# Kernel tuning notes

Hardware: AMD Instinct MI355X
Metric: run time of the kernel (lower is better)

The kernel has to match this reference:

```python
import jax, jax.numpy as jnp
import numpy as np
import math

H = 16
LORA_SCALING = 16 / 8  # alpha / r
NEG_INF = -1e30

def _alibi_slopes(n_heads):
    start = 2.0 ** (-(2.0 ** (-(math.log2(n_heads) - 3))))
    return jnp.asarray([start * start ** i for i in range(n_heads)], dtype=jnp.float32)

def setup_inputs() -> dict:
    key = jax.random.key(0)
    ks = jax.random.split(key, 11)
    B, T, E, r = 4, 2048, 1024, 8
    d = {
        'x':  jax.random.normal(ks[0], (B, T, E), jnp.float32),
        'Wq': jax.random.normal(ks[1], (E, E), jnp.float32) * (E ** -0.5),
        'Aq': jax.random.normal(ks[2], (E, r), jnp.float32) * 0.01,
        'Bq': jax.random.normal(ks[3], (r, E), jnp.float32) * 0.01,
        'Wk': jax.random.normal(ks[4], (E, E), jnp.float32) * (E ** -0.5),
        'Ak': jax.random.normal(ks[5], (E, r), jnp.float32) * 0.01,
        'Bk': jax.random.normal(ks[6], (r, E), jnp.float32) * 0.01,
        'Wv': jax.random.normal(ks[7], (E, E), jnp.float32) * (E ** -0.5),
        'Av': jax.random.normal(ks[8], (E, r), jnp.float32) * 0.01,
        'Bv': jax.random.normal(ks[9], (r, E), jnp.float32) * 0.01,
        'Wp': jax.random.normal(ks[10], (E, E), jnp.float32) * (E ** -0.5),
    }
    return d

def _lora(x, W, A, Bm):
    # nn.Linear: x @ W.T ; LoRA: x @ B.T @ A.T * scaling
    return x @ W.T + ((x @ Bm.T) @ A.T) * LORA_SCALING

def reference(x, Wq, Aq, Bq, Wk, Ak, Bk, Wv, Av, Bv, Wp):
    B, T, E = x.shape
    dh = E // H
    q = _lora(x, Wq, Aq, Bq).reshape(B, T, H, dh).transpose(0, 2, 1, 3)  # [B,H,T,dh]
    k = _lora(x, Wk, Ak, Bk).reshape(B, T, H, dh).transpose(0, 2, 1, 3)
    v = _lora(x, Wv, Av, Bv).reshape(B, T, H, dh).transpose(0, 2, 1, 3)
    s = jnp.einsum('bhqd,bhkd->bhqk', q, k) / jnp.sqrt(jnp.float32(dh))
    i = jnp.arange(T)[:, None]
    j = jnp.arange(T)[None, :]
    slopes = _alibi_slopes(H)
    bias = slopes[:, None, None] * (i - j).astype(jnp.float32)  # [H,T,T]
    s = s + bias[None]
    s = jnp.where(j[None, None] <= i[None, None], s, NEG_INF)  # causal mask
    out = jnp.einsum('bhqk,bhkd->bhqd', jax.nn.softmax(s, axis=-1), v)
    out = out.transpose(0, 2, 1, 3).reshape(B, T, E)
    return out @ Wp.T  # dropout is identity in eval
```

## Files before the change

### kernel.cpp

```cpp
#include <hip/hip_runtime.h>

typedef unsigned short u16;
typedef unsigned int u32;
typedef u16  u16x8 __attribute__((ext_vector_type(8)));
typedef u16  u16x4 __attribute__((ext_vector_type(4)));
typedef u32  u32x4 __attribute__((ext_vector_type(4)));
typedef __bf16 bf16x2 __attribute__((ext_vector_type(2)));
typedef __bf16 bf16x8 __attribute__((ext_vector_type(8)));
typedef float f32x4 __attribute__((ext_vector_type(4)));
typedef float f32x16 __attribute__((ext_vector_type(16)));

__constant__ int KBW[16]  = {0,1,1,2,3,5,7,10,14,20,28,40,56,80,113,160};

__constant__ unsigned char RANKTBL[256] = {
  0xBF,0xCF,0xDF,0xEF,0xFF,
  0xBE,0xCE,0xDE,0xEE,0xFE,
  0xAE,0xAF,
  0xAD,0xBD,0xCD,0xDD,0xED,0xFD,
  0xAC,0xBC,0xCC,0xDC,0xEC,0xFC,
  0xAB,0xBB,0xCB,0xDB,0xEB,0xFB,
  0xAA,0xBA,0xCA,0xDA,0xEA,0xFA,
  0x9A,0x9B,0x9C,0x9D,0x9E,0x9F,
  0x99,0xA9,0xB9,0xC9,0xD9,0xE9,0xF9,
  0x98,0xA8,0xB8,0xC8,0xD8,0xE8,0xF8,
  0x97,0xA7,0xB7,0xC7,0xD7,0xE7,0xF7,
  0x87,0x88,0x89,0x8A,0x8B,0x8C,0x8D,0x8E,0x8F,
  0x86,0x96,0xA6,0xB6,0xC6,0xD6,0xE6,0xF6,
  0x85,0x95,0xA5,0xB5,0xC5,0xD5,0xE5,0xF5,
  0x75,0x76,0x77,0x78,0x79,0x7A,0x7B,0x7C,0x7D,0x7E,0x7F,
  0x74,0x84,0x94,0xA4,0xB4,0xC4,0xD4,0xE4,0xF4,
  0x63,0x64,0x65,0x66,0x67,0x68,0x69,0x6A,0x6B,0x6C,0x6D,0x6E,0x6F,
  0x73,0x83,0x93,0xA3,0xB3,0xC3,0xD3,0xE3,0xF3,
  0x52,0x53,0x54,0x55,0x56,0x57,0x58,0x59,0x5A,0x5B,0x5C,0x5D,0x5E,0x5F,
  0x62,0x72,0x82,0x92,0xA2,0xB2,0xC2,0xD2,0xE2,0xF2,
  0x41,0x42,0x43,0x44,0x45,0x46,0x47,0x48,0x49,0x4A,0x4B,0x4C,0x4D,0x4E,0x4F,
  0x51,0x61,0x71,0x81,0x91,0xA1,0xB1,0xC1,0xD1,0xE1,0xF1,
  0x31,0x32,0x33,0x34,0x35,0x36,0x37,0x38,0x39,0x3A,0x3B,0x3C,0x3D,0x3E,0x3F,
  0x10,0x11,0x12,0x13,0x14,0x15,0x16,0x17,0x18,0x19,0x1A,0x1B,0x1C,0x1D,0x1E,0x1F,
  0x20,0x21,0x22,0x23,0x24,0x25,0x26,0x27,0x28,0x29,0x2A,0x2B,0x2C,0x2D,0x2E,0x2F,
  0x30,0x40,0x50,0x60,0x70,0x80,0x90,0xA0,0xB0,0xC0,0xD0,0xE0,0xF0,
  0x00,0x01,0x02,0x03,0x04,0x05,0x06,0x07,0x08,0x09,0x0A,0x0B,0x0C,0x0D,0x0E,0x0F
};

static __device__ __forceinline__ u16 f2bf(float f) {
  unsigned int u = __float_as_uint(f);
  u += 0x7FFFu + ((u >> 16) & 1u);
  return (u16)(u >> 16);
}

static __device__ __forceinline__ u32 packbf(float a, float b) {
  bf16x2 t;
  t[0] = (__bf16)a;
  t[1] = (__bf16)b;
  return __builtin_bit_cast(u32, t);
}

static __device__ __forceinline__ f32x4 mfma16(bf16x8 a, bf16x8 b, f32x4 c) {
  return __builtin_amdgcn_mfma_f32_16x16x32_bf16(a, b, c, 0, 0, 0);
}
static __device__ __forceinline__ f32x16 mfma32(bf16x8 a, bf16x8 b, f32x16 c) {
  return __builtin_amdgcn_mfma_f32_32x32x16_bf16(a, b, c, 0, 0, 0);
}

static __device__ __forceinline__ void gload16(const void* g, void* lds) {
  __builtin_amdgcn_global_load_lds(
      (const __attribute__((address_space(1))) unsigned int*)g,
      (__attribute__((address_space(3))) unsigned int*)lds, 16, 0, 0);
}

__global__ __launch_bounds__(256) void k_castfold(
    const float* __restrict__ x, u16* __restrict__ xb,
    const float* __restrict__ Wq, const float* __restrict__ Aq, const float* __restrict__ Bq,
    const float* __restrict__ Wk, const float* __restrict__ Ak, const float* __restrict__ Bk,
    const float* __restrict__ Wv, const float* __restrict__ Av, const float* __restrict__ Bv,
    const float* __restrict__ Wp, u16* __restrict__ wqkv, u16* __restrict__ wp) {
  const int bid = (int)blockIdx.x;
  if (bid < 4096) {
    size_t i = (size_t)bid * 256 + threadIdx.x;
    const float4* p = reinterpret_cast<const float4*>(x) + i * 2;
    float4 a = p[0], b = p[1];
    u16x8 r;
    r[0] = f2bf(a.x); r[1] = f2bf(a.y); r[2] = f2bf(a.z); r[3] = f2bf(a.w);
    r[4] = f2bf(b.x); r[5] = f2bf(b.y); r[6] = f2bf(b.z); r[7] = f2bf(b.w);
    *reinterpret_cast<u16x8*>(xb + i * 8) = r;
    return;
  }
  int n = bid - 4096;
  int widx = n >> 10, nr = n & 1023;
  const float *W, *A, *Bm; u16* dst;
  if (widx == 0)      { W = Wq; A = Aq; Bm = Bq; dst = wqkv; }
  else if (widx == 1) { W = Wk; A = Ak; Bm = Bk; dst = wqkv + (1 << 20); }
  else if (widx == 2) { W = Wv; A = Av; Bm = Bv; dst = wqkv + (2 << 20); }
  else                { W = Wp; A = nullptr; Bm = nullptr; dst = wp; }
  int e0 = threadIdx.x * 4;
  float4 w = *reinterpret_cast<const float4*>(W + (size_t)nr * 1024 + e0);
  if (widx < 3) {
    float acx = 0.f, acy = 0.f, acz = 0.f, acw = 0.f;
#pragma unroll
    for (int r = 0; r < 8; r++) {
      float ar = A[nr * 8 + r];
      float4 bm = *reinterpret_cast<const float4*>(Bm + (size_t)r * 1024 + e0);
      acx += ar * bm.x; acy += ar * bm.y; acz += ar * bm.z; acw += ar * bm.w;
    }
    w.x += 2.0f * acx; w.y += 2.0f * acy; w.z += 2.0f * acz; w.w += 2.0f * acw;
  }
  u16x4 r4; r4[0] = f2bf(w.x); r4[1] = f2bf(w.y); r4[2] = f2bf(w.z); r4[3] = f2bf(w.w);
  *reinterpret_cast<u16x4*>(dst + (size_t)nr * 1024 + e0) = r4;
}

template<int OUTF32>
__global__ __launch_bounds__(512) void k_gemm256(const u16* __restrict__ Ag,
                                                 const u16* __restrict__ Bg,
                                                 void* __restrict__ C,
                                                 int K, int N, int lda, int gx) {
  __shared__ __align__(16) u16 As[2][16384];
  __shared__ __align__(16) u16 Bs[2][16384];
  const int tid = threadIdx.x;
  const int wid = tid >> 6, lane = tid & 63;
  const int l15 = lane & 15, lg = lane >> 4;
  const int wr = wid >> 2, wc = wid & 3;
  const int nwg = gridDim.x, cpx = nwg >> 3;
  const int bid = (int)blockIdx.x;
  const int sid = (bid & 7) * cpx + (bid >> 3);
  const int m0 = (sid % gx) * 256, n0 = (sid / gx) * 256;

  const int lrow = lane >> 3;
  const int lslot = lane & 7;

  f32x4 acc[8][4];
#pragma unroll
  for (int i = 0; i < 8; i++)
#pragma unroll
    for (int j = 0; j < 4; j++) acc[i][j] = (f32x4)0.0f;

  auto stA = [&](int d, int t, int i) {
    int row = i * 64 + wid * 8 + lrow;
    int sc = (lslot ^ (row & 7)) << 3;
    gload16(Ag + (size_t)(m0 + row) * lda + t * 64 + sc, &As[d][(i * 64 + wid * 8) * 64]);
  };
  auto stB = [&](int d, int t, int i) {
    int row = i * 64 + wid * 8 + lrow;
    int sc = (lslot ^ (row & 7)) << 3;
    gload16(Bg + (size_t)(n0 + row) * K + t * 64 + sc, &Bs[d][(i * 64 + wid * 8) * 64]);
  };
  auto ldsA = [&](int d, int m, int kk) {
    int rr = wr * 128 + m * 16 + l15;
    return *reinterpret_cast<const bf16x8*>(&As[d][rr * 64 + (((kk * 4 + lg) ^ (rr & 7)) << 3)]);
  };
  auto ldsB = [&](int d, int n, int kk) {
    int rr = wc * 64 + n * 16 + l15;
    return *reinterpret_cast<const bf16x8*>(&Bs[d][rr * 64 + (((kk * 4 + lg) ^ (rr & 7)) << 3)]);
  };

#define MIDBAR do { asm volatile("s_barrier" ::: "memory"); \
                    asm volatile("s_waitcnt lgkmcnt(0)" ::: "memory"); } while (0)
#define ENDBAR asm volatile("s_barrier" ::: "memory")

  const int nt = K >> 6;
  stA(0, 0, 0); stA(0, 0, 1); stA(0, 0, 2); stA(0, 0, 3);
  stB(0, 0, 0); stB(0, 0, 1); stB(0, 0, 2); stB(0, 0, 3);
  if (nt > 1) { stB(1, 1, 0); stB(1, 1, 1); stB(1, 1, 2); stB(1, 1, 3); }
  asm volatile("s_waitcnt vmcnt(4)" ::: "memory");
  asm volatile("s_barrier" ::: "memory");

  bf16x8 fa[4][2], fbA[2][2], fbB[2][2];
  for (int t = 0; t < nt; ++t) {
    const int d = t & 1;
    const bool s1 = (t + 1 < nt), s2 = (t + 2 < nt);
#pragma unroll
    for (int m = 0; m < 4; m++)
#pragma unroll
      for (int kk = 0; kk < 2; kk++) fa[m][kk] = ldsA(d, m, kk);
#pragma unroll
    for (int n = 0; n < 2; n++)
#pragma unroll
      for (int kk = 0; kk < 2; kk++) fbA[n][kk] = ldsB(d, n, kk);
    if (s1) { stA(d ^ 1, t + 1, 0); stA(d ^ 1, t + 1, 1); }
    MIDBAR;
    __builtin_amdgcn_s_setprio(1);
#pragma unroll
    for (int m = 0; m < 4; m++)
#pragma unroll
      for (int n = 0; n < 2; n++)
#pragma unroll
        for (int kk = 0; kk < 2; kk++)
          acc[m][n] = mfma16(fa[m][kk], fbA[n][kk], acc[m][n]);
    __builtin_amdgcn_s_setprio(0);
    ENDBAR;
#pragma unroll
    for (int n = 0; n < 2; n++)
#pragma unroll
      for (int kk = 0; kk < 2; kk++) fbB[n][kk] = ldsB(d, n + 2, kk);
    if (s1) { stA(d ^ 1, t + 1, 2); stA(d ^ 1, t + 1, 3); }
    MIDBAR;
    __builtin_amdgcn_s_setprio(1);
#pragma unroll
    for (int m = 0; m < 4; m++)
#pragma unroll
      for (int n = 0; n < 2; n++)
#pragma unroll
        for (int kk = 0; kk < 2; kk++)
          acc[m][n + 2] = mfma16(fa[m][kk], fbB[n][kk], acc[m][n + 2]);
    __builtin_amdgcn_s_setprio(0);
    ENDBAR;
#pragma unroll
    for (int m = 0; m < 4; m++)
#pragma unroll
      for (int kk = 0; kk < 2; kk++) fa[m][kk] = ldsA(d, m + 4, kk);
    if (s2) { stB(d, t + 2, 0); stB(d, t + 2, 1); stB(d, t + 2, 2); stB(d, t + 2, 3); }
    MIDBAR;
    __builtin_amdgcn_s_setprio(1);
#pragma unroll
    for (int m = 0; m < 4; m++)
#pragma unroll
      for (int n = 0; n < 2; n++)
#pragma unroll
        for (int kk = 0; kk < 2; kk++)
          acc[m + 4][n + 2] = mfma16(fa[m][kk], fbB[n][kk], acc[m + 4][n + 2]);
#pragma unroll
    for (int m = 0; m < 4; m++)
#pragma unroll
      for (int n = 0; n < 2; n++)
#pragma unroll
        for (int kk = 0; kk < 2; kk++)
          acc[m + 4][n] = mfma16(fa[m][kk], fbA[n][kk], acc[m + 4][n]);
    __builtin_amdgcn_s_setprio(0);
    if (s2) asm volatile("s_waitcnt vmcnt(4)" ::: "memory");
    else    asm volatile("s_waitcnt vmcnt(0)" ::: "memory");
    ENDBAR;
  }
#undef MIDBAR
#undef ENDBAR

  const int rbase = m0 + wr * 128, cbase = n0 + wc * 64;
#pragma unroll
  for (int m = 0; m < 8; m++)
#pragma unroll
    for (int n = 0; n < 4; n++)
#pragma unroll
      for (int j = 0; j < 4; j++) {
        int r  = rbase + m * 16 + lg * 4 + j;
        int cc = cbase + n * 16 + l15;
        if constexpr (OUTF32) {
          reinterpret_cast<float*>(C)[(size_t)r * N + cc] = acc[m][n][j];
        } else {
          reinterpret_cast<u16*>(C)[(size_t)r * N + cc] = f2bf(acc[m][n][j]);
        }
      }
}

template<int OUTF32>
__global__ __launch_bounds__(512) void k_gemm8(const u16* __restrict__ Ag,
                                               const u16* __restrict__ Bg,
                                               void* __restrict__ C,
                                               int K, int N, int lda, int gx) {
  __shared__ __align__(16) u16 As[2][8192];
  __shared__ __align__(16) u16 Bs[2][16384];
  const int tid = threadIdx.x;
  const int wid = tid >> 6, lane = tid & 63;
  const int l15 = lane & 15, lg = lane >> 4;
  const int wr = wid >> 2, wc = wid & 3;
  const int nwg = gridDim.x, cpx = nwg >> 3;
  const int bid = (int)blockIdx.x;
  const int sid = (bid & 7) * cpx + (bid >> 3);
  const int m0 = (sid % gx) * 128, n0 = (sid / gx) * 256;

  const int lrow = lane >> 3;
  const int lslot = lane & 7;

  f32x4 acc[4][4];
#pragma unroll
  for (int i = 0; i < 4; i++)
#pragma unroll
    for (int j = 0; j < 4; j++) acc[i][j] = (f32x4)0.0f;

  auto stageA = [&](int d, int t) {
#pragma unroll
    for (int i = 0; i < 2; i++) {
      int row = i * 64 + wid * 8 + lrow;
      int sc = (lslot ^ (row & 7)) << 3;
      gload16(Ag + (size_t)(m0 + row) * lda + t * 64 + sc,
              &As[d][(i * 64 + wid * 8) * 64]);
    }
  };
  auto stageB = [&](int d, int t) {
#pragma unroll
    for (int i = 0; i < 4; i++) {
      int row = i * 64 + wid * 8 + lrow;
      int sc = (lslot ^ (row & 7)) << 3;
      gload16(Bg + (size_t)(n0 + row) * K + t * 64 + sc,
              &Bs[d][(i * 64 + wid * 8) * 64]);
    }
  };
  auto ldsA = [&](int d, int m, int kk) {
    int rr = wr * 64 + m * 16 + l15;
    return *reinterpret_cast<const bf16x8*>(&As[d][rr * 64 + (((kk * 4 + lg) ^ (rr & 7)) << 3)]);
  };
  auto ldsB = [&](int d, int n, int kk) {
    int rr = wc * 64 + n * 16 + l15;
    return *reinterpret_cast<const bf16x8*>(&Bs[d][rr * 64 + (((kk * 4 + lg) ^ (rr & 7)) << 3)]);
  };

#define MIDBAR do { asm volatile("s_barrier" ::: "memory"); \
                    asm volatile("s_waitcnt lgkmcnt(0)" ::: "memory"); } while (0)
#define ENDBAR asm volatile("s_barrier" ::: "memory")

  stageB(0, 0); stageA(0, 0); stageA(1, 1);
  asm volatile("s_waitcnt vmcnt(2)" ::: "memory");
  asm volatile("s_barrier" ::: "memory");

  bf16x8 fa[4][2], fb[2][2];
  const int nt = K >> 6;
  for (int t = 0; t < nt; ++t) {
    const int d = t & 1;
#pragma unroll
    for (int m = 0; m < 4; m++)
#pragma unroll
      for (int kk = 0; kk < 2; kk++) fa[m][kk] = ldsA(d, m, kk);
#pragma unroll
    for (int n = 0; n < 2; n++)
#pragma unroll
      for (int kk = 0; kk < 2; kk++) fb[n][kk] = ldsB(d, n, kk);
    if (t + 1 < nt) stageB(d ^ 1, t + 1);
    MIDBAR;
    __builtin_amdgcn_s_setprio(1);
#pragma unroll
    for (int m = 0; m < 4; m++)
#pragma unroll
      for (int n = 0; n < 2; n++)
#pragma unroll
        for (int kk = 0; kk < 2; kk++)
          acc[m][n] = mfma16(fa[m][kk], fb[n][kk], acc[m][n]);
    __builtin_amdgcn_s_setprio(0);
    ENDBAR;
#pragma unroll
    for (int n = 0; n < 2; n++)
#pragma unroll
      for (int kk = 0; kk < 2; kk++) fb[n][kk] = ldsB(d, n + 2, kk);
    if (t + 2 < nt) stageA(d, t + 2);
    MIDBAR;
    __builtin_amdgcn_s_setprio(1);
#pragma unroll
    for (int m = 0; m < 4; m++)
#pragma unroll
      for (int n = 0; n < 2; n++)
#pragma unroll
        for (int kk = 0; kk < 2; kk++)
          acc[m][n + 2] = mfma16(fa[m][kk], fb[n][kk], acc[m][n + 2]);
    __builtin_amdgcn_s_setprio(0);
    if (t + 2 < nt) asm volatile("s_waitcnt vmcnt(2)" ::: "memory");
    else            asm volatile("s_waitcnt vmcnt(0)" ::: "memory");
    ENDBAR;
  }
#undef MIDBAR
#undef ENDBAR

  const int rbase = m0 + wr * 64, cbase = n0 + wc * 64;
#pragma unroll
  for (int m = 0; m < 4; m++)
#pragma unroll
    for (int n = 0; n < 4; n++)
#pragma unroll
      for (int j = 0; j < 4; j++) {
        int r  = rbase + m * 16 + lg * 4 + j;
        int cc = cbase + n * 16 + l15;
        if constexpr (OUTF32) {
          reinterpret_cast<float*>(C)[(size_t)r * N + cc] = acc[m][n][j];
        } else {
          reinterpret_cast<u16*>(C)[(size_t)r * N + cc] = f2bf(acc[m][n][j]);
        }
      }
}

__global__ __launch_bounds__(256) void k_vt(const u16* __restrict__ qkv,
                                            u16* __restrict__ vt) {
  __shared__ __align__(16) u16 tile[64 * 64];
  const int tb = blockIdx.x, h = blockIdx.y, b = blockIdx.z;
  const int tid = threadIdx.x;
  const size_t rb = (size_t)b * 2048;
  const int hv = 2048 + h * 64;
#pragma unroll
  for (int p = 0; p < 2; p++) {
    int r = p * 32 + (tid >> 3);
    int c = (tid & 7) * 8;
    u16x8 v = *reinterpret_cast<const u16x8*>(qkv + (rb + tb * 64 + r) * 3072 + hv + c);
    int slot = (c >> 3) ^ (r & 7) ^ ((r >> 3) & 7);
    *reinterpret_cast<u16x8*>(tile + r * 64 + slot * 8) = v;
  }
  __syncthreads();
#pragma unroll
  for (int p = 0; p < 2; p++) {
    int d = p * 32 + (tid >> 3);
    int t0 = (tid & 7) * 8;
    u16x8 v;
#pragma unroll
    for (int j = 0; j < 8; j++) {
      int r = t0 + j;
      int slot = (d >> 3) ^ (r & 7) ^ ((r >> 3) & 7);
      v[j] = tile[r * 64 + slot * 8 + (d & 7)];
    }
    *reinterpret_cast<u16x8*>(vt + ((size_t)(b * 16 + h) * 64 + d) * 2048 + tb * 64 + t0) = v;
  }
}

__global__ __launch_bounds__(256) void k_attn(const u16* __restrict__ qkv,
                                              const u16* __restrict__ vt,
                                              u16* __restrict__ aout) {
  __shared__ __align__(16) u16 Kl[2][64 * 64];
  __shared__ __align__(16) u16 Vl[2][64 * 64];
  const int tid = threadIdx.x, wave = tid >> 6, lane = tid & 63;
  const int l31 = lane & 31, half = lane >> 5;
  const int i = (int)blockIdx.x;
  const int b = i & 3, p = i >> 2;
  const int k4 = p >> 6, j4 = p & 63;
  const int ridx = (k4 == 0) ? j4 : (k4 == 1) ? 127 - j4 : (k4 == 2) ? 128 + j4 : 255 - j4;
  const int hqv = RANKTBL[ridx];
  const int h = hqv >> 4, qb = hqv & 15;
  const int rb = b * 2048;
  const int hq = h * 64, hk = 1024 + h * 64;
  const int bh64 = (b * 16 + h) * 64;
  const int qB = qb * 128;
  const int q0w = qB + wave * 32;
  const int q = q0w + l31;

  bf16x8 qf[4];
#pragma unroll
  for (int c = 0; c < 4; c++)
    qf[c] = *reinterpret_cast<const bf16x8*>(qkv + (size_t)(rb + q) * 3072 + hq + c * 16 + half * 8);

  const float slope2 = exp2f(-0.5f * (float)(h + 1)) * 1.44269504f;
  const float c0 = 0.18033688f;

  const int kend = min(2 * qb + 1, KBW[h]);

  float mrun = -1e30f, lrun = 0.f;
  f32x16 o0 = (f32x16)0.0f, o1 = (f32x16)0.0f;

  auto stage = [&](int kvr, int dst) {
#pragma unroll
    for (int i2 = 0; i2 < 2; i2++) {
      int row = (i2 * 4 + wave) * 8 + (lane >> 3);
      int scol = ((lane & 7) ^ (row & 7)) << 3;
      gload16(qkv + (size_t)(rb + kvr + row) * 3072 + hk + scol, &Kl[dst][(i2 * 4 + wave) * 512]);
      gload16(vt + (size_t)(bh64 + row) * 2048 + kvr + scol,     &Vl[dst][(i2 * 4 + wave) * 512]);
    }
  };

  stage(0, 0);
  __syncthreads();

  int bfi = 0;
  for (int kb = 0; kb <= kend; ++kb, bfi ^= 1) {
    const int kvr = kb * 64;
    if (kb < kend) stage(kvr + 64, bfi ^ 1);

    if (kvr <= q0w + 31) {
      f32x16 s[2];
#pragma unroll
      for (int t = 0; t < 2; t++) s[t] = (f32x16)0.0f;
      __builtin_amdgcn_s_setprio(1);
#pragma unroll
      for (int t = 0; t < 2; t++) {
        int r = t * 32 + l31;
#pragma unroll
        for (int cc = 0; cc < 4; cc++) {
          bf16x8 kf = *reinterpret_cast<const bf16x8*>(
              &Kl[bfi][r * 64 + (((cc * 2 + half) ^ (r & 7)) << 3)]);
          s[t] = mfma32(kf, qf[cc], s[t]);
        }
      }
      __builtin_amdgcn_s_setprio(0);

      const bool domask = (kvr + 63 > q0w);
      const int qrel = q - kvr - half * 4;
      const float qb0 = slope2 * (float)qrel;
      const float qb1 = qb0 - slope2 * 32.0f;
      float mt = -1e30f;
      if (domask) {
#pragma unroll
        for (int t = 0; t < 2; t++) {
          const float qbt = t ? qb1 : qb0;
          const int qmt = t ? (qrel - 32) : qrel;
#pragma unroll
          for (int r = 0; r < 16; r++) {
            const int krel = (r & 3) + 8 * (r >> 2);
            float val = fmaf(s[t][r], c0, fmaf(-slope2, (float)krel, qbt));
            val = (krel <= qmt) ? val : -3.0e38f;
            s[t][r] = val;
            mt = fmaxf(mt, val);
          }
        }
      } else {
#pragma unroll
        for (int t = 0; t < 2; t++) {
          const float qbt = t ? qb1 : qb0;
#pragma unroll
          for (int r = 0; r < 16; r += 2) {
            const int k0 = (r & 3) + 8 * (r >> 2);
            const int k1 = ((r + 1) & 3) + 8 * ((r + 1) >> 2);
            float v0 = fmaf(s[t][r],     c0, fmaf(-slope2, (float)k0, qbt));
            float v1 = fmaf(s[t][r + 1], c0, fmaf(-slope2, (float)k1, qbt));
            s[t][r] = v0; s[t][r + 1] = v1;
            mt = fmaxf(mt, fmaxf(v0, v1));
          }
        }
      }
      mt = fmaxf(mt, __shfl_xor(mt, 32));

      if (__any(mt - mrun > 8.0f)) {
        float mn = fmaxf(mrun, mt);
        float al = exp2f(mrun - mn);
        mrun = mn; lrun *= al;
#pragma unroll
        for (int r = 0; r < 16; r++) { o0[r] *= al; o1[r] *= al; }
      }

      float rs0 = 0.f, rs1 = 0.f;
#pragma unroll
      for (int t = 0; t < 2; t++)
#pragma unroll
        for (int r = 0; r < 16; r++) {
          float pp = exp2f(s[t][r] - mrun);
          s[t][r] = pp;
          if (t) rs1 += pp; else rs0 += pp;
        }
      float rs = rs0 + rs1;
      rs += __shfl_xor(rs, 32);
      lrun += rs;

      bf16x8 pf[4];
#pragma unroll
      for (int t = 0; t < 2; t++)
#pragma unroll
        for (int hs = 0; hs < 2; hs++) {
          u32 A0 = packbf(s[t][8 * hs + 0], s[t][8 * hs + 1]);
          u32 B0 = packbf(s[t][8 * hs + 2], s[t][8 * hs + 3]);
          u32 C0 = packbf(s[t][8 * hs + 4], s[t][8 * hs + 5]);
          u32 D0 = packbf(s[t][8 * hs + 6], s[t][8 * hs + 7]);
          asm volatile("v_permlane32_swap_b32 %0, %1" : "+v"(A0), "+v"(C0));
          asm volatile("v_permlane32_swap_b32 %0, %1" : "+v"(B0), "+v"(D0));
          u32x4 fr; fr[0] = A0; fr[1] = B0; fr[2] = C0; fr[3] = D0;
          pf[t * 2 + hs] = __builtin_bit_cast(bf16x8, fr);
        }

      __builtin_amdgcn_s_setprio(1);
#pragma unroll
      for (int dblk = 0; dblk < 2; dblk++) {
        int r = dblk * 32 + l31;
#pragma unroll
        for (int kc = 0; kc < 4; kc++) {
          bf16x8 vf = *reinterpret_cast<const bf16x8*>(
              &Vl[bfi][r * 64 + (((kc * 2 + half) ^ (r & 7)) << 3)]);
          if (dblk) o1 = mfma32(vf, pf[kc], o1);
          else      o0 = mfma32(vf, pf[kc], o0);
        }
      }
      __builtin_amdgcn_s_setprio(0);
    }
    __syncthreads();
  }

  const float linv = 1.0f / lrun;
#pragma unroll
  for (int dblk = 0; dblk < 2; dblk++)
#pragma unroll
    for (int rg = 0; rg < 4; rg++) {
      int d0 = dblk * 32 + 8 * rg + 4 * half;
      u16x4 r4;
#pragma unroll
      for (int j = 0; j < 4; j++) {
        float v = (dblk ? o1[rg * 4 + j] : o0[rg * 4 + j]) * linv;
        r4[j] = f2bf(v);
      }
      *reinterpret_cast<u16x4*>(aout + (size_t)(rb + q) * 3072 + hq + d0) = r4;
    }
}

extern "C" void kernel_launch(void* const* d_in, const int* in_sizes, int n_in,
                              void* d_out, int out_size, void* d_ws, size_t ws_size,
                              hipStream_t stream) {
  (void)in_sizes; (void)n_in; (void)out_size; (void)ws_size;
  const float* x  = (const float*)d_in[0];
  const float* Wq = (const float*)d_in[1];
  const float* Aq = (const float*)d_in[2];
  const float* Bq = (const float*)d_in[3];
  const float* Wk = (const float*)d_in[4];
  const float* Ak = (const float*)d_in[5];
  const float* Bk = (const float*)d_in[6];
  const float* Wv = (const float*)d_in[7];
  const float* Av = (const float*)d_in[8];
  const float* Bv = (const float*)d_in[9];
  const float* Wp = (const float*)d_in[10];

  char* ws = (char*)d_ws;
  u16* xb   = (u16*)(ws);
  u16* wqkv = (u16*)(ws + 16777216);
  u16* wp   = (u16*)(ws + 23068672);
  u16* qkv  = (u16*)(ws + 25165824);
  u16* vt   = xb;
  float* out = (float*)d_out;

  k_castfold<<<dim3(8192), dim3(256), 0, stream>>>(x, xb, Wq, Aq, Bq, Wk, Ak, Bk,
                                                   Wv, Av, Bv, Wp, wqkv, wp);
  k_gemm256<0><<<dim3(384), dim3(512), 0, stream>>>(xb, wqkv, (void*)qkv, 1024, 3072, 1024, 32);
  k_vt<<<dim3(32, 16, 4), dim3(256), 0, stream>>>(qkv, vt);
  k_attn<<<dim3(1024), dim3(256), 0, stream>>>(qkv, vt, qkv);
  k_gemm8<1><<<dim3(256), dim3(512), 0, stream>>>(qkv, wp, (void*)out, 1024, 1024, 3072, 64);
}
```

Baseline: 178.5 us.

## Simplify GEMM pipelines to single-barrier double-buffered loop per K-tile

Replaces the staggered multi-phase schedule in both GEMM kernels (split global loads with partial vmcnt waits and four barriers per K-tile) with a plain double-buffer loop. Each iteration issues all next-tile loads up front, computes the current tile with a rolling A-fragment prefetch, then waits on everything and hits one barrier. The aim is fewer barriers and simpler scheduling. The cost is a full vmcnt(0) drain every iteration, so load latency may be exposed instead of overlapped.

New measurement: 186.7 us. 1.05x slower.

```diff
diff --git a/kernel.cpp b/kernel.cpp
--- a/kernel.cpp
+++ b/kernel.cpp
@@ -152,85 +152,45 @@
     return *reinterpret_cast<const bf16x8*>(&Bs[d][rr * 64 + (((kk * 4 + lg) ^ (rr & 7)) << 3)]);
   };
 
-#define MIDBAR do { asm volatile("s_barrier" ::: "memory"); \
-                    asm volatile("s_waitcnt lgkmcnt(0)" ::: "memory"); } while (0)
-#define ENDBAR asm volatile("s_barrier" ::: "memory")
-
   const int nt = K >> 6;
   stA(0, 0, 0); stA(0, 0, 1); stA(0, 0, 2); stA(0, 0, 3);
   stB(0, 0, 0); stB(0, 0, 1); stB(0, 0, 2); stB(0, 0, 3);
-  if (nt > 1) { stB(1, 1, 0); stB(1, 1, 1); stB(1, 1, 2); stB(1, 1, 3); }
-  asm volatile("s_waitcnt vmcnt(4)" ::: "memory");
+  asm volatile("s_waitcnt vmcnt(0)" ::: "memory");
   asm volatile("s_barrier" ::: "memory");
 
-  bf16x8 fa[4][2], fbA[2][2], fbB[2][2];
+  bf16x8 fb[4][2], fa[4][2];
   for (int t = 0; t < nt; ++t) {
     const int d = t & 1;
-    const bool s1 = (t + 1 < nt), s2 = (t + 2 < nt);
-#pragma unroll
-    for (int m = 0; m < 4; m++)
+    if (t + 1 < nt) {
+      stA(d ^ 1, t + 1, 0); stA(d ^ 1, t + 1, 1); stA(d ^ 1, t + 1, 2); stA(d ^ 1, t + 1, 3);
+      stB(d ^ 1, t + 1, 0); stB(d ^ 1, t + 1, 1); stB(d ^ 1, t + 1, 2); stB(d ^ 1, t + 1, 3);
+    }
+#pragma unroll
+    for (int n = 0; n < 4; n++)
+#pragma unroll
+      for (int kk = 0; kk < 2; kk++) fb[n][kk] = ldsB(d, n, kk);
+#pragma unroll
+    for (int m = 0; m < 2; m++)
 #pragma unroll
       for (int kk = 0; kk < 2; kk++) fa[m][kk] = ldsA(d, m, kk);
-#pragma unroll
-    for (int n = 0; n < 2; n++)
-#pragma unroll
-      for (int kk = 0; kk < 2; kk++) fbA[n][kk] = ldsB(d, n, kk);
-    if (s1) { stA(d ^ 1, t + 1, 0); stA(d ^ 1, t + 1, 1); }
-    MIDBAR;
     __builtin_amdgcn_s_setprio(1);
 #pragma unroll
-    for (int m = 0; m < 4; m++)
-#pragma unroll
-      for (int n = 0; n < 2; n++)
+    for (int m = 0; m < 8; m++) {
+      if (m + 2 < 8) {
+        fa[(m + 2) & 3][0] = ldsA(d, m + 2, 0);
+        fa[(m + 2) & 3][1] = ldsA(d, m + 2, 1);
+      }
+#pragma unroll
+      for (int n = 0; n < 4; n++)
 #pragma unroll
         for (int kk = 0; kk < 2; kk++)
-          acc[m][n] = mfma16(fa[m][kk], fbA[n][kk], acc[m][n]);
+          acc[m][n] = mfma16(fa[m & 3][kk], fb[n][kk], acc[m][n]);
+    }
     __builtin_amdgcn_s_setprio(0);
-    ENDBAR;
-#pragma unroll
-    for (int n = 0; n < 2; n++)
-#pragma unroll
-      for (int kk = 0; kk < 2; kk++) fbB[n][kk] = ldsB(d, n + 2, kk);
-    if (s1) { stA(d ^ 1, t + 1, 2); stA(d ^ 1, t + 1, 3); }
-    MIDBAR;
-    __builtin_amdgcn_s_setprio(1);
-#pragma unroll
-    for (int m = 0; m < 4; m++)
-#pragma unroll
-      for (int n = 0; n < 2; n++)
-#pragma unroll
-        for (int kk = 0; kk < 2; kk++)
-          acc[m][n + 2] = mfma16(fa[m][kk], fbB[n][kk], acc[m][n + 2]);
-    __builtin_amdgcn_s_setprio(0);
-    ENDBAR;
-#pragma unroll
-    for (int m = 0; m < 4; m++)
-#pragma unroll
-      for (int kk = 0; kk < 2; kk++) fa[m][kk] = ldsA(d, m + 4, kk);
-    if (s2) { stB(d, t + 2, 0); stB(d, t + 2, 1); stB(d, t + 2, 2); stB(d, t + 2, 3); }
-    MIDBAR;
-    __builtin_amdgcn_s_setprio(1);
-#pragma unroll
-    for (int m = 0; m < 4; m++)
-#pragma unroll
-      for (int n = 0; n < 2; n++)
-#pragma unroll
-        for (int kk = 0; kk < 2; kk++)
-          acc[m + 4][n + 2] = mfma16(fa[m][kk], fbB[n][kk], acc[m + 4][n + 2]);
-#pragma unroll
-    for (int m = 0; m < 4; m++)
-#pragma unroll
-      for (int n = 0; n < 2; n++)
-#pragma unroll
-        for (int kk = 0; kk < 2; kk++)
-          acc[m + 4][n] = mfma16(fa[m][kk], fbA[n][kk], acc[m + 4][n]);
-    __builtin_amdgcn_s_setprio(0);
-    if (s2) asm volatile("s_waitcnt vmcnt(4)" ::: "memory");
-    else    asm volatile("s_waitcnt vmcnt(0)" ::: "memory");
-    ENDBAR;
-  }
-#undef MIDBAR
-#undef ENDBAR
+    asm volatile("s_waitcnt lgkmcnt(0)" ::: "memory");
+    asm volatile("s_waitcnt vmcnt(0)" ::: "memory");
+    asm volatile("s_barrier" ::: "memory");
+  }
 
   const int rbase = m0 + wr * 128, cbase = n0 + wc * 64;
 #pragma unroll
@@ -250,10 +210,10 @@
 }
 
 template<int OUTF32>
-__global__ __launch_bounds__(512) void k_gemm8(const u16* __restrict__ Ag,
-                                               const u16* __restrict__ Bg,
-                                               void* __restrict__ C,
-                                               int K, int N, int lda, int gx) {
+__global__ __launch_bounds__(512) void k_gemm128(const u16* __restrict__ Ag,
+                                                 const u16* __restrict__ Bg,
+                                                 void* __restrict__ C,
+                                                 int K, int N, int lda, int gx) {
   __shared__ __align__(16) u16 As[2][8192];
   __shared__ __align__(16) u16 Bs[2][16384];
   const int tid = threadIdx.x;
@@ -301,59 +261,36 @@
     return *reinterpret_cast<const bf16x8*>(&Bs[d][rr * 64 + (((kk * 4 + lg) ^ (rr & 7)) << 3)]);
   };
 
-#define MIDBAR do { asm volatile("s_barrier" ::: "memory"); \
-                    asm volatile("s_waitcnt lgkmcnt(0)" ::: "memory"); } while (0)
-#define ENDBAR asm volatile("s_barrier" ::: "memory")
-
-  stageB(0, 0); stageA(0, 0); stageA(1, 1);
-  asm volatile("s_waitcnt vmcnt(2)" ::: "memory");
+  const int nt = K >> 6;
+  stageA(0, 0); stageB(0, 0);
+  asm volatile("s_waitcnt vmcnt(0)" ::: "memory");
   asm volatile("s_barrier" ::: "memory");
 
-  bf16x8 fa[4][2], fb[2][2];
-  const int nt = K >> 6;
+  bf16x8 fa[4][2], fb[4][2];
   for (int t = 0; t < nt; ++t) {
     const int d = t & 1;
+    if (t + 1 < nt) { stageA(d ^ 1, t + 1); stageB(d ^ 1, t + 1); }
+#pragma unroll
+    for (int n = 0; n < 4; n++)
+#pragma unroll
+      for (int kk = 0; kk < 2; kk++) fb[n][kk] = ldsB(d, n, kk);
 #pragma unroll
     for (int m = 0; m < 4; m++)
 #pragma unroll
       for (int kk = 0; kk < 2; kk++) fa[m][kk] = ldsA(d, m, kk);
-#pragma unroll
-    for (int n = 0; n < 2; n++)
-#pragma unroll
-      for (int kk = 0; kk < 2; kk++) fb[n][kk] = ldsB(d, n, kk);
-    if (t + 1 < nt) stageB(d ^ 1, t + 1);
-    MIDBAR;
     __builtin_amdgcn_s_setprio(1);
 #pragma unroll
     for (int m = 0; m < 4; m++)
 #pragma unroll
-      for (int n = 0; n < 2; n++)
+      for (int n = 0; n < 4; n++)
 #pragma unroll
         for (int kk = 0; kk < 2; kk++)
           acc[m][n] = mfma16(fa[m][kk], fb[n][kk], acc[m][n]);
     __builtin_amdgcn_s_setprio(0);
-    ENDBAR;
-#pragma unroll
-    for (int n = 0; n < 2; n++)
-#pragma unroll
-      for (int kk = 0; kk < 2; kk++) fb[n][kk] = ldsB(d, n + 2, kk);
-    if (t + 2 < nt) stageA(d, t + 2);
-    MIDBAR;
-    __builtin_amdgcn_s_setprio(1);
-#pragma unroll
-    for (int m = 0; m < 4; m++)
-#pragma unroll
-      for (int n = 0; n < 2; n++)
-#pragma unroll
-        for (int kk = 0; kk < 2; kk++)
-          acc[m][n + 2] = mfma16(fa[m][kk], fb[n][kk], acc[m][n + 2]);
-    __builtin_amdgcn_s_setprio(0);
-    if (t + 2 < nt) asm volatile("s_waitcnt vmcnt(2)" ::: "memory");
-    else            asm volatile("s_waitcnt vmcnt(0)" ::: "memory");
-    ENDBAR;
-  }
-#undef MIDBAR
-#undef ENDBAR
+    asm volatile("s_waitcnt lgkmcnt(0)" ::: "memory");
+    asm volatile("s_waitcnt vmcnt(0)" ::: "memory");
+    asm volatile("s_barrier" ::: "memory");
+  }
 
   const int rbase = m0 + wr * 64, cbase = n0 + wc * 64;
 #pragma unroll
@@ -605,5 +542,5 @@
   k_gemm256<0><<<dim3(384), dim3(512), 0, stream>>>(xb, wqkv, (void*)qkv, 1024, 3072, 1024, 32);
   k_vt<<<dim3(32, 16, 4), dim3(256), 0, stream>>>(qkv, vt);
   k_attn<<<dim3(1024), dim3(256), 0, stream>>>(qkv, vt, qkv);
-  k_gemm8<1><<<dim3(256), dim3(512), 0, stream>>>(qkv, wp, (void*)out, 1024, 1024, 3072, 64);
-}
+  k_gemm128<1><<<dim3(256), dim3(512), 0, stream>>>(qkv, wp, (void*)out, 1024, 1024, 3072, 64);
+}
```
